# Kernel tuning notes

Hardware: AMD Instinct MI355X
Metric: run time of the kernel (lower is better)

Reference implementation:

```python
import jax, jax.numpy as jnp
import numpy as np


def setup_inputs() -> dict:
    key = jax.random.key(0)
    k1, k2, k3 = jax.random.split(key, 3)
    B, S, D, N = 2, 2048, 1024, 16
    H = D // N  # head_dim = 64
    x = jax.random.normal(k1, (B, S, D), dtype=jnp.float32)
    W_qkv = jax.random.normal(k2, (N, D, 3 * H), dtype=jnp.float32) / np.sqrt(D).astype(np.float32)
    W_out = jax.random.normal(k3, (N, H, D), dtype=jnp.float32) / np.sqrt(D).astype(np.float32)
    return {"x": x, "W_qkv": W_qkv, "W_out": W_out}


def reference(x, W_qkv, W_out):
    B, S, D = x.shape
    head_dim = W_qkv.shape[-1] // 3
    # QKV projection per head: [B, N, S, 3*H]
    qkv = jnp.einsum('bsd,ndh->bnsh', x, W_qkv)
    q, k, v = jnp.split(qkv, 3, axis=-1)  # each [B, N, S, H]
    scale = jnp.asarray(1.0 / np.sqrt(head_dim), dtype=x.dtype)
    attn = jnp.einsum('bnqh,bnkh->bnqk', q, k) * scale  # [B, N, S, S]
    # causal mask: -1e10 above the diagonal (matches buffer in original)
    mask = jnp.asarray(-1e10, dtype=x.dtype) * (1.0 - jnp.tril(jnp.ones((S, S), dtype=x.dtype)))
    attn = jax.nn.softmax(attn + mask, axis=-1)
    out = jnp.einsum('bnqk,bnkh->bnqh', attn, v)  # [B, N, S, H]
    # faithful to original: raw row-major reshape [B,N,S,H] -> [B, N*H, S]
    out = out.reshape(B, -1, S)
    # faithful to original einsum: d kept, n and h summed over W_out
    return jnp.einsum('bds,nhd->bsd', out, W_out)
```

## Files before the change

### kernel.cpp

```cpp
#include <hip/hip_runtime.h>
#include <hip/hip_bf16.h>

#define B_ 2
#define S_ 2048
#define D_ 1024
#define N_ 16
#define H_ 64

typedef unsigned short u16;
typedef unsigned int u32;
typedef __bf16 bf16x8 __attribute__((ext_vector_type(8)));
typedef u16 u16x8 __attribute__((ext_vector_type(8)));
typedef u32 u32x2 __attribute__((ext_vector_type(2)));
typedef u32 u32x4 __attribute__((ext_vector_type(4)));
typedef float f4v __attribute__((ext_vector_type(4)));

__device__ __forceinline__ u16 f2b(float f) {
    u32 u = __builtin_bit_cast(u32, f);
    u32 r = (u + 0x7FFFu + ((u >> 16) & 1u)) >> 16;
    return (u16)r;
}
__device__ __forceinline__ bf16x8 asbf(u16x8 v) { return __builtin_bit_cast(bf16x8, v); }
__device__ __forceinline__ u32 cvtpk(float a, float b) {
    u32 r;
    asm("v_cvt_pk_bf16_f32 %0, %1, %2" : "=v"(r) : "v"(a), "v"(b));
    return r;
}
__device__ __forceinline__ void gload16(const u16* g, u16* l) {
    __builtin_amdgcn_global_load_lds((const __attribute__((address_space(1))) void*)g,
                                     (__attribute__((address_space(3))) void*)l, 16, 0, 0);
}

__global__ __launch_bounds__(256) void k_setup(const float* __restrict__ x,
                                               const float* __restrict__ w,
                                               const float* __restrict__ Wout,
                                               u16* __restrict__ xb,
                                               u16* __restrict__ wt,
                                               float* __restrict__ wsum) {
    __shared__ float T[64][65];
    const int bid = blockIdx.x;
    const int t = threadIdx.x;
    if (bid < 2048) {
        size_t i = ((size_t)bid * 256 + t) * 8;
        float4 f0 = *(const float4*)(x + i);
        float4 f1 = *(const float4*)(x + i + 4);
        u16x8 o;
        o[0] = f2b(f0.x); o[1] = f2b(f0.y); o[2] = f2b(f0.z); o[3] = f2b(f0.w);
        o[4] = f2b(f1.x); o[5] = f2b(f1.y); o[6] = f2b(f1.z); o[7] = f2b(f1.w);
        *(u16x8*)(xb + i) = o;
    } else if (bid < 2816) {
        const int v = bid - 2048;
        const int n = v / 48, rem = v % 48;
        const int jt = rem >> 4, d0 = (rem & 15) * 64;
        const int j0 = jt * 64;
        const float sc = (jt == 0) ? 0.125f * 1.44269504089f : 1.0f;
#pragma unroll
        for (int rep = 0; rep < 4; ++rep) {
            int vv = t + rep * 256;
            int row = vv >> 4, c4 = vv & 15;
            float4 f = *(const float4*)(w + ((size_t)(n * 1024 + d0 + row)) * 192 + j0 + c4 * 4);
            T[row][c4 * 4 + 0] = f.x * sc;
            T[row][c4 * 4 + 1] = f.y * sc;
            T[row][c4 * 4 + 2] = f.z * sc;
            T[row][c4 * 4 + 3] = f.w * sc;
        }
        __syncthreads();
#pragma unroll
        for (int rep = 0; rep < 2; ++rep) {
            int c = t + rep * 256;
            int j = c >> 3, db = c & 7;
            u16x8 o;
#pragma unroll
            for (int e = 0; e < 8; ++e) o[e] = f2b(T[db * 8 + e][j]);
            *(u16x8*)(wt + ((size_t)(n * 192 + j0 + j)) * 1024 + d0 + db * 8) = o;
        }
    } else {
        const int bx = bid - 2816;
        const int dd = t & 15, rr = t >> 4;
        const int d = bx * 16 + dd;
        float s = 0.f;
        for (int r = rr * 64; r < rr * 64 + 64; ++r) s += Wout[(size_t)r * 1024 + d];
        float* red = &T[0][0];
        red[rr * 17 + dd] = s;
        __syncthreads();
        if (rr == 0) {
            float tt = 0.f;
#pragma unroll
            for (int k = 0; k < 16; ++k) tt += red[k * 17 + dd];
            wsum[d] = tt;
        }
    }
}

__global__ __launch_bounds__(512) void k_qkv(const u16* __restrict__ xb,
                                             const u16* __restrict__ wt,
                                             u16* __restrict__ qbuf,
                                             u16* __restrict__ kbuf,
                                             u16* __restrict__ vt) {
    __shared__ u16 As[128 * 64];
    __shared__ u16 Bst[192 * 64];
    const int st = blockIdx.x, n = blockIdx.y;
    const int t = threadIdx.x;
    const int w = t >> 6, lane = t & 63, hi2 = lane >> 4, lo4 = lane & 15;
    const int wm = w >> 2, wn = w & 3;

    const int l8 = lane >> 3;
    const int l7s = ((lane & 7) ^ l8) * 8;
    const u16* AgL = xb + (size_t)(st * 128 + w * 16 + l8) * 1024 + l7s;
    u16* AdL = As + w * 16 * 64;
    const u16* BgL = wt + (size_t)(n * 192 + w * 24 + l8) * 1024 + l7s;
    u16* BdL = Bst + w * 24 * 64;

    f4v acc[4][3];
#pragma unroll
    for (int i = 0; i < 4; ++i)
#pragma unroll
        for (int j = 0; j < 3; ++j) acc[i][j] = (f4v){0.f, 0.f, 0.f, 0.f};

    const int rsw = (lo4 & 7) << 3;
    for (int kk = 0; kk < 16; ++kk) {
        __syncthreads();
        const int ko = kk * 64;
        gload16(AgL + ko, AdL);
        gload16(AgL + ko + (size_t)8 * 1024, AdL + 8 * 64);
        gload16(BgL + ko, BdL);
        gload16(BgL + ko + (size_t)8 * 1024, BdL + 8 * 64);
        gload16(BgL + ko + (size_t)16 * 1024, BdL + 16 * 64);
        __syncthreads();
        bf16x8 fa[4][2];
#pragma unroll
        for (int ms = 0; ms < 4; ++ms) {
            const u16* ar = As + (wm * 64 + ms * 16 + lo4) * 64;
            fa[ms][0] = asbf(*(const u16x8*)(ar + ((hi2 * 8) ^ rsw)));
            fa[ms][1] = asbf(*(const u16x8*)(ar + ((hi2 * 8 + 32) ^ rsw)));
        }
        __builtin_amdgcn_s_setprio(1);
#pragma unroll
        for (int fj = 0; fj < 3; ++fj) {
            const u16* br = Bst + (wn * 48 + fj * 16 + lo4) * 64;
            bf16x8 fb0 = asbf(*(const u16x8*)(br + ((hi2 * 8) ^ rsw)));
            bf16x8 fb1 = asbf(*(const u16x8*)(br + ((hi2 * 8 + 32) ^ rsw)));
#pragma unroll
            for (int ms = 0; ms < 4; ++ms) {
                acc[ms][fj] = __builtin_amdgcn_mfma_f32_16x16x32_bf16(fa[ms][0], fb0, acc[ms][fj], 0, 0, 0);
                acc[ms][fj] = __builtin_amdgcn_mfma_f32_16x16x32_bf16(fa[ms][1], fb1, acc[ms][fj], 0, 0, 0);
            }
        }
        __builtin_amdgcn_s_setprio(0);
    }

    const int b = st >> 4, s128 = (st & 15) * 128;
    u16* Cs = As;
#pragma unroll
    for (int sec = 0; sec < 3; ++sec) {
        __syncthreads();
#pragma unroll
        for (int fj = 0; fj < 3; ++fj) {
            const int base = wn * 48 + fj * 16;
            if ((base >> 6) == sec) {
                const int col = base - sec * 64 + lo4;
#pragma unroll
                for (int ms = 0; ms < 4; ++ms)
#pragma unroll
                    for (int r = 0; r < 4; ++r)
                        Cs[(wm * 64 + ms * 16 + hi2 * 4 + r) * 64 + col] = f2b(acc[ms][fj][r]);
            }
        }
        __syncthreads();
        if (sec == 2) {
            const int h = t & 63, sb = t >> 6;
            u16x8 o0, o1;
#pragma unroll
            for (int e = 0; e < 8; ++e) o0[e] = Cs[(sb * 16 + e) * 64 + h];
#pragma unroll
            for (int e = 0; e < 8; ++e) o1[e] = Cs[(sb * 16 + 8 + e) * 64 + h];
            u16* dst = vt + ((size_t)(b * 16 + n) * 64 + h) * 2048 + s128 + sb * 16;
            *(u16x8*)dst = o0;
            *(u16x8*)(dst + 8) = o1;
        } else {
            const int row = t >> 2, off = (t & 3) * 16;
            u16* dst = (sec == 0) ? qbuf : kbuf;
            dst += ((size_t)(b * 16 + n) * 2048 + s128 + row) * 64 + off;
            *(u16x8*)dst = *(const u16x8*)(Cs + row * 64 + off);
            *(u16x8*)(dst + 8) = *(const u16x8*)(Cs + row * 64 + off + 8);
        }
    }
}

__global__ __launch_bounds__(512) void k_attn(const u16* __restrict__ qbuf,
                                              const u16* __restrict__ kbuf,
                                              const u16* __restrict__ vt,
                                              const float* __restrict__ wsum,
                                              float* __restrict__ out) {
    __shared__ u16 SMEM[16384];
    u16* Ks = SMEM;
    u16* Vs = SMEM + 8192;
    const int id = blockIdx.x;
    const int bn = id & 31;
    const int qx = id >> 5;
    const int qb = (qx < 8) ? (15 - 2 * qx) : (2 * (qx - 8));
    const int t = threadIdx.x;
    const int w = t >> 6, lane = t & 63, hi2 = lane >> 4, lo4 = lane & 15;

    const int q = qb * 128 + w * 16 + lo4;
    const u16* Qp = qbuf + ((size_t)bn * 2048 + q) * 64;
    bf16x8 bq0 = asbf(*(const u16x8*)(Qp + hi2 * 8));
    bf16x8 bq1 = asbf(*(const u16x8*)(Qp + 32 + hi2 * 8));

    u16x8 ones_u;
#pragma unroll
    for (int e = 0; e < 8; ++e) ones_u[e] = 0x3F80;
    const bf16x8 ones = asbf(ones_u);

    const int srow = t >> 3, so = t & 7;
    const u16* Kg = kbuf + (size_t)bn * 2048 * 64 + (size_t)srow * 64 + so * 8;
    const u16* Vg = vt + (size_t)bn * 64 * 2048 + (size_t)srow * 2048 + so * 8;
    const int ssw = (srow & 7) << 3;
    const int ksoff = srow * 64 + ((so * 8) ^ ssw);
    const int vsb = 32 * (so >> 2) + 16 * (so & 1) + 4 * ((so >> 1) & 1);
    const int vo0 = srow * 64 + ((vsb + 0) ^ ssw);
    const int vo1 = srow * 64 + ((vsb + 8) ^ ssw);

    f4v accO[4];
#pragma unroll
    for (int i = 0; i < 4; ++i) accO[i] = (f4v){0.f, 0.f, 0.f, 0.f};
    f4v accL = (f4v){0.f, 0.f, 0.f, 0.f};

    const int rsw = (lo4 & 7) << 3;
    const int npair = qb + 1;

    u16x8 krA = *(const u16x8*)(Kg);
    u16x8 krB = *(const u16x8*)(Kg + 4096);
    u16x8 vrA = *(const u16x8*)(Vg);
    u16x8 vrB = *(const u16x8*)(Vg + 64);

    for (int pair = 0; pair < npair; ++pair) {
        __syncthreads();
        *(u16x8*)(Ks + ksoff) = krA;
        *(u16x8*)(Ks + 4096 + ksoff) = krB;
        {
            u32x4 va = __builtin_bit_cast(u32x4, vrA);
            u32x4 vb = __builtin_bit_cast(u32x4, vrB);
            *(u32x2*)(Vs + vo0) = (u32x2){va[0], va[1]};
            *(u32x2*)(Vs + vo1) = (u32x2){va[2], va[3]};
            *(u32x2*)(Vs + 4096 + vo0) = (u32x2){vb[0], vb[1]};
            *(u32x2*)(Vs + 4096 + vo1) = (u32x2){vb[2], vb[3]};
        }
        if (pair + 1 < npair) {
            const size_t ko = (size_t)(pair + 1) * 8192;
            krA = *(const u16x8*)(Kg + ko);
            krB = *(const u16x8*)(Kg + ko + 4096);
            vrA = *(const u16x8*)(Vg + (pair + 1) * 128);
            vrB = *(const u16x8*)(Vg + (pair + 1) * 128 + 64);
        }
        __syncthreads();

#pragma unroll
        for (int sub = 0; sub < 2; ++sub) {
            const int kb = 2 * pair + sub;
            const u16* Kc = Ks + sub * 4096;
            const u16* Vc = Vs + sub * 4096;

            f4v s4[4];
#pragma unroll
            for (int i = 0; i < 4; ++i) s4[i] = (f4v){0.f, 0.f, 0.f, 0.f};
            __builtin_amdgcn_s_setprio(1);
#pragma unroll
            for (int fi = 0; fi < 4; ++fi) {
                const u16* kr = Kc + (fi * 16 + lo4) * 64;
                bf16x8 ka0 = asbf(*(const u16x8*)(kr + ((hi2 * 8) ^ rsw)));
                bf16x8 ka1 = asbf(*(const u16x8*)(kr + ((hi2 * 8 + 32) ^ rsw)));
                s4[fi] = __builtin_amdgcn_mfma_f32_16x16x32_bf16(ka0, bq0, s4[fi], 0, 0, 0);
                s4[fi] = __builtin_amdgcn_mfma_f32_16x16x32_bf16(ka1, bq1, s4[fi], 0, 0, 0);
            }
            __builtin_amdgcn_s_setprio(0);

            if (kb >= 2 * qb) {
#pragma unroll
                for (int fi = 0; fi < 4; ++fi)
#pragma unroll
                    for (int r = 0; r < 4; ++r) {
                        int kvg = kb * 64 + fi * 16 + hi2 * 4 + r;
                        if (kvg > q) s4[fi][r] = -3.0e38f;
                    }
            }

#pragma unroll
            for (int fi = 0; fi < 4; ++fi)
#pragma unroll
                for (int r = 0; r < 4; ++r)
                    s4[fi][r] = __builtin_exp2f(s4[fi][r]);

            u32x4 p0 = {cvtpk(s4[0][0], s4[0][1]), cvtpk(s4[0][2], s4[0][3]),
                        cvtpk(s4[1][0], s4[1][1]), cvtpk(s4[1][2], s4[1][3])};
            u32x4 p1 = {cvtpk(s4[2][0], s4[2][1]), cvtpk(s4[2][2], s4[2][3]),
                        cvtpk(s4[3][0], s4[3][1]), cvtpk(s4[3][2], s4[3][3])};
            bf16x8 pb0 = __builtin_bit_cast(bf16x8, p0);
            bf16x8 pb1 = __builtin_bit_cast(bf16x8, p1);

            __builtin_amdgcn_s_setprio(1);
#pragma unroll
            for (int fh = 0; fh < 4; ++fh) {
                const u16* vrw = Vc + (fh * 16 + lo4) * 64;
                bf16x8 va0 = asbf(*(const u16x8*)(vrw + ((hi2 * 8) ^ rsw)));
                bf16x8 va1 = asbf(*(const u16x8*)(vrw + ((32 + hi2 * 8) ^ rsw)));
                accO[fh] = __builtin_amdgcn_mfma_f32_16x16x32_bf16(va0, pb0, accO[fh], 0, 0, 0);
                accO[fh] = __builtin_amdgcn_mfma_f32_16x16x32_bf16(va1, pb1, accO[fh], 0, 0, 0);
            }
            accL = __builtin_amdgcn_mfma_f32_16x16x32_bf16(ones, pb0, accL, 0, 0, 0);
            accL = __builtin_amdgcn_mfma_f32_16x16x32_bf16(ones, pb1, accL, 0, 0, 0);
            __builtin_amdgcn_s_setprio(0);
        }
    }

    const float l = accL[0];

    __syncthreads();
    float* Osh = (float*)SMEM;
    {
        float inv = 1.f / l;
        const int orl = w * 16 + lo4;
        const int osw = (lo4 & 7) << 2;
        float* Or = Osh + orl * 64;
#pragma unroll
        for (int fh = 0; fh < 4; ++fh) {
            f4v o;
#pragma unroll
            for (int r = 0; r < 4; ++r) o[r] = accO[fh][r] * inv;
            *(f4v*)(Or + ((fh * 16 + hi2 * 4) ^ osw)) = o;
        }
    }
    __syncthreads();
    {
        const int b = bn >> 4, n = bn & 15;
        const int d0 = n * 64 + qb * 4;
        float4 wv = *(const float4*)(wsum + d0);
#pragma unroll
        for (int rep = 0; rep < 4; ++rep) {
            int p = rep * 512 + t;
            int h = p & 63, tt = p >> 6;
            const int key = (tt & 7) << 2;
            const int hc = h ^ key;
            float4 o;
            o.x = Osh[(tt)*64 + hc] * wv.x;
            o.y = Osh[(32 + tt) * 64 + hc] * wv.y;
            o.z = Osh[(64 + tt) * 64 + hc] * wv.z;
            o.w = Osh[(96 + tt) * 64 + hc] * wv.w;
            *(float4*)(out + ((size_t)b * 2048 + p) * 1024 + d0) = o;
        }
    }
}

extern "C" void kernel_launch(void* const* d_in, const int* in_sizes, int n_in,
                              void* d_out, int out_size, void* d_ws, size_t ws_size,
                              hipStream_t stream) {
    const float* x = (const float*)d_in[0];
    const float* Wqkv = (const float*)d_in[1];
    const float* Wout = (const float*)d_in[2];
    float* out = (float*)d_out;

    char* p = (char*)d_ws;
    float* wsum = (float*)p; p += 4096;
    u16* xb = (u16*)p; p += (size_t)4096 * 1024 * 2;
    u16* wt = (u16*)p; p += (size_t)16 * 192 * 1024 * 2;
    u16* qb_ = (u16*)p; p += (size_t)32 * 2048 * 64 * 2;
    u16* kb_ = (u16*)p; p += (size_t)32 * 2048 * 64 * 2;
    u16* vt_ = (u16*)p; p += (size_t)32 * 2048 * 64 * 2;

    k_setup<<<2880, 256, 0, stream>>>(x, Wqkv, Wout, xb, wt, wsum);
    k_qkv<<<dim3(32, 16), 512, 0, stream>>>(xb, wt, qb_, kb_, vt_);
    k_attn<<<512, 512, 0, stream>>>(qb_, kb_, vt_, wsum, out);
}
```

Measured before the change: 81.39 us.

## Stream K/V tiles into double-buffered LDS with direct global-to-LDS loads

The attention kernel now loads K and V tiles with global_load_lds straight into shared memory, instead of staging them through registers and storing them to LDS. LDS is double-buffered, so the next pair of tiles is prefetched while the current one is consumed, and one barrier per iteration is dropped. The projection kernel writes the transposed V in a permuted column order, and the K source columns are XOR-swizzled, so the direct copies land in the layout the MFMA reads expect. The cost is twice the LDS per block, which may limit occupancy. Correctness depends on the asynchronous LDS writes being complete at each remaining barrier.

```diff
diff --git a/kernel.cpp b/kernel.cpp
--- a/kernel.cpp
+++ b/kernel.cpp
@@ -11,6 +11,7 @@
 typedef unsigned int u32;
 typedef __bf16 bf16x8 __attribute__((ext_vector_type(8)));
 typedef u16 u16x8 __attribute__((ext_vector_type(8)));
+typedef u16 u16x4 __attribute__((ext_vector_type(4)));
 typedef u32 u32x2 __attribute__((ext_vector_type(2)));
 typedef u32 u32x4 __attribute__((ext_vector_type(4)));
 typedef float f4v __attribute__((ext_vector_type(4)));
@@ -174,9 +175,12 @@
             for (int e = 0; e < 8; ++e) o0[e] = Cs[(sb * 16 + e) * 64 + h];
 #pragma unroll
             for (int e = 0; e < 8; ++e) o1[e] = Cs[(sb * 16 + 8 + e) * 64 + h];
-            u16* dst = vt + ((size_t)(b * 16 + n) * 64 + h) * 2048 + s128 + sb * 16;
-            *(u16x8*)dst = o0;
-            *(u16x8*)(dst + 8) = o1;
+            u16* dstb = vt + ((size_t)(b * 16 + n) * 64 + h) * 2048 + s128 +
+                        ((sb >> 2) << 6) + (((sb & 3) >> 1) << 5) + ((sb & 1) << 2);
+            *(u16x4*)(dstb + 0) = (u16x4){o0[0], o0[1], o0[2], o0[3]};
+            *(u16x4*)(dstb + 8) = (u16x4){o0[4], o0[5], o0[6], o0[7]};
+            *(u16x4*)(dstb + 16) = (u16x4){o1[0], o1[1], o1[2], o1[3]};
+            *(u16x4*)(dstb + 24) = (u16x4){o1[4], o1[5], o1[6], o1[7]};
         } else {
             const int row = t >> 2, off = (t & 3) * 16;
             u16* dst = (sec == 0) ? qbuf : kbuf;
@@ -192,9 +196,9 @@
                                               const u16* __restrict__ vt,
                                               const float* __restrict__ wsum,
                                               float* __restrict__ out) {
-    __shared__ u16 SMEM[16384];
+    __shared__ u16 SMEM[32768];
     u16* Ks = SMEM;
-    u16* Vs = SMEM + 8192;
+    u16* Vs = SMEM + 16384;
     const int id = blockIdx.x;
     const int bn = id & 31;
     const int qx = id >> 5;
@@ -212,14 +216,12 @@
     for (int e = 0; e < 8; ++e) ones_u[e] = 0x3F80;
     const bf16x8 ones = asbf(ones_u);
 
-    const int srow = t >> 3, so = t & 7;
-    const u16* Kg = kbuf + (size_t)bn * 2048 * 64 + (size_t)srow * 64 + so * 8;
-    const u16* Vg = vt + (size_t)bn * 64 * 2048 + (size_t)srow * 2048 + so * 8;
-    const int ssw = (srow & 7) << 3;
-    const int ksoff = srow * 64 + ((so * 8) ^ ssw);
-    const int vsb = 32 * (so >> 2) + 16 * (so & 1) + 4 * ((so >> 1) & 1);
-    const int vo0 = srow * 64 + ((vsb + 0) ^ ssw);
-    const int vo1 = srow * 64 + ((vsb + 8) ^ ssw);
+    const int lr = lane >> 3;
+    const int lcs = ((lane & 7) ^ lr) * 8;
+    const u16* KgL = kbuf + (size_t)bn * 131072 + (size_t)(w * 8 + lr) * 64 + lcs;
+    const u16* VgL = vt + (size_t)bn * 131072 + (size_t)(w * 8 + lr) * 2048 + lcs;
+    u16* Kd = Ks + w * 512;
+    u16* Vd = Vs + w * 512;
 
     f4v accO[4];
 #pragma unroll
@@ -229,37 +231,29 @@
     const int rsw = (lo4 & 7) << 3;
     const int npair = qb + 1;
 
-    u16x8 krA = *(const u16x8*)(Kg);
-    u16x8 krB = *(const u16x8*)(Kg + 4096);
-    u16x8 vrA = *(const u16x8*)(Vg);
-    u16x8 vrB = *(const u16x8*)(Vg + 64);
+    gload16(KgL, Kd);
+    gload16(KgL + 4096, Kd + 4096);
+    gload16(VgL, Vd);
+    gload16(VgL + 64, Vd + 4096);
 
     for (int pair = 0; pair < npair; ++pair) {
         __syncthreads();
-        *(u16x8*)(Ks + ksoff) = krA;
-        *(u16x8*)(Ks + 4096 + ksoff) = krB;
-        {
-            u32x4 va = __builtin_bit_cast(u32x4, vrA);
-            u32x4 vb = __builtin_bit_cast(u32x4, vrB);
-            *(u32x2*)(Vs + vo0) = (u32x2){va[0], va[1]};
-            *(u32x2*)(Vs + vo1) = (u32x2){va[2], va[3]};
-            *(u32x2*)(Vs + 4096 + vo0) = (u32x2){vb[0], vb[1]};
-            *(u32x2*)(Vs + 4096 + vo1) = (u32x2){vb[2], vb[3]};
-        }
+        const int beta = pair & 1;
         if (pair + 1 < npair) {
+            const int nb = (beta ^ 1) * 8192;
             const size_t ko = (size_t)(pair + 1) * 8192;
-            krA = *(const u16x8*)(Kg + ko);
-            krB = *(const u16x8*)(Kg + ko + 4096);
-            vrA = *(const u16x8*)(Vg + (pair + 1) * 128);
-            vrB = *(const u16x8*)(Vg + (pair + 1) * 128 + 64);
-        }
-        __syncthreads();
+            const int vo = (pair + 1) * 128;
+            gload16(KgL + ko, Kd + nb);
+            gload16(KgL + ko + 4096, Kd + nb + 4096);
+            gload16(VgL + vo, Vd + nb);
+            gload16(VgL + vo + 64, Vd + nb + 4096);
+        }
 
 #pragma unroll
         for (int sub = 0; sub < 2; ++sub) {
             const int kb = 2 * pair + sub;
-            const u16* Kc = Ks + sub * 4096;
-            const u16* Vc = Vs + sub * 4096;
+            const u16* Kc = Ks + beta * 8192 + sub * 4096;
+            const u16* Vc = Vs + beta * 8192 + sub * 4096;
 
             f4v s4[4];
 #pragma unroll
```

Measured after the change: 82.78 us. Within noise of the previous version (+1.7%).
